# Kernel optimization log

Measured on AMD Instinct MI355X. Metric: run time of the kernel, lower is better.

The kernel has to match this reference:

```python
import jax, jax.numpy as jnp
import numpy as np

N_NODES = 100000
N_EDGES = 1600000
D_FEAT = 128
ALPHA = 0.1
K_STEPS = 10


def setup_inputs() -> dict:
    key = jax.random.key(0)
    k1, k2, k3 = jax.random.split(key, 3)
    x = jax.random.normal(k1, (N_NODES, D_FEAT), dtype=jnp.float32)
    edge_index = jax.random.randint(k2, (2, N_EDGES), 0, N_NODES, dtype=jnp.int64)
    edge_vals = jax.random.uniform(k3, (N_EDGES,), dtype=jnp.float32)
    return {"x": x, "edge_index": edge_index, "edge_vals": edge_vals}


def _spmm(edge_index, edge_vals, h, n_nodes):
    # out[i] = sum_j A[i, j] * h[j]; row = edge_index[0], col = edge_index[1]
    row, col = edge_index[0], edge_index[1]
    msgs = edge_vals[:, None] * h[col]  # [E, d]
    return jax.ops.segment_sum(msgs, row, num_segments=n_nodes)


def reference(x, edge_index, edge_vals):
    # APPNP propagation: h <- (1 - alpha) * A @ h + alpha * x, K steps.
    # dropout=0.0 -> dropout is the identity (as in the torch module default).
    def body(_, h):
        return (1.0 - ALPHA) * _spmm(edge_index, edge_vals, h, N_NODES) + ALPHA * x

    return jax.lax.fori_loop(0, K_STEPS, body, x)
```

## Files before the change

### kernel.cpp

```cpp
#include <hip/hip_runtime.h>


#define N_NODES 100000
#define N_EDGES 1600000
#define D_FEAT  128
#define ALPHA   0.1f
#define K_STEPS 10
#define MAXDEG  64

#define SCAN_ELEMS 512
#define SCAN_NBLK  ((N_NODES + SCAN_ELEMS - 1) / SCAN_ELEMS)

static __device__ __forceinline__ float bf2f(unsigned u16) {
    return __uint_as_float(u16 << 16);
}
static __device__ __forceinline__ unsigned f2bf(float f) {
    unsigned u = __float_as_uint(f);
    return (u + 0x7fffu + ((u >> 16) & 1u)) >> 16;
}


__global__ __launch_bounds__(256) void scatter_padded(const int* __restrict__ rows,
                                                      const int* __restrict__ cols,
                                                      const float* __restrict__ w,
                                                      int* __restrict__ cnt,
                                                      int2* __restrict__ csrp) {
    int e = blockIdx.x * 256 + threadIdx.x;
    if (e < N_EDGES) {
        int r = rows[e];
        int pos = atomicAdd(&cnt[r], 1);
        if (pos < MAXDEG) {
            int2 cw;
            cw.x = cols[e];
            cw.y = __float_as_int((1.0f - ALPHA) * w[e]);
            csrp[((size_t)r << 6) + pos] = cw;
        }
    }
}


__global__ __launch_bounds__(256) void hist_kernel(const int* __restrict__ rows,
                                                   int* __restrict__ deg) {
    int e = blockIdx.x * 256 + threadIdx.x;
    if (e < N_EDGES) atomicAdd(&deg[rows[e]], 1);
}

__global__ __launch_bounds__(256) void scan_partial(const int* __restrict__ deg,
                                                    int* __restrict__ partial) {
    __shared__ int s[256];
    int b = blockIdx.x, t = threadIdx.x;
    int i0 = b * SCAN_ELEMS + t * 2;
    int v0 = (i0 < N_NODES) ? deg[i0] : 0;
    int v1 = (i0 + 1 < N_NODES) ? deg[i0 + 1] : 0;
    s[t] = v0 + v1;
    __syncthreads();
    for (int off = 128; off > 0; off >>= 1) {
        if (t < off) s[t] += s[t + off];
        __syncthreads();
    }
    if (t == 0) partial[b] = s[0];
}

__global__ __launch_bounds__(256) void scan_top(int* __restrict__ partial) {
    __shared__ int s[256];
    int t = threadIdx.x;
    s[t] = (t < SCAN_NBLK) ? partial[t] : 0;
    __syncthreads();
    for (int off = 1; off < 256; off <<= 1) {
        int v = (t >= off) ? s[t - off] : 0;
        __syncthreads();
        s[t] += v;
        __syncthreads();
    }
    if (t < SCAN_NBLK) partial[t] = (t == 0) ? 0 : s[t - 1];
}

__global__ __launch_bounds__(256) void scan_final(int* __restrict__ deg_cursor,
                                                  const int* __restrict__ partial,
                                                  int* __restrict__ row_ptr) {
    __shared__ int s[256];
    int b = blockIdx.x, t = threadIdx.x;
    int i0 = b * SCAN_ELEMS + t * 2;
    int v0 = (i0 < N_NODES) ? deg_cursor[i0] : 0;
    int v1 = (i0 + 1 < N_NODES) ? deg_cursor[i0 + 1] : 0;
    int pair = v0 + v1;
    s[t] = pair;
    __syncthreads();
    for (int off = 1; off < 256; off <<= 1) {
        int v = (t >= off) ? s[t - off] : 0;
        __syncthreads();
        s[t] += v;
        __syncthreads();
    }
    int ex = partial[b] + s[t] - pair;
    if (i0 < N_NODES)     { row_ptr[i0] = ex;          deg_cursor[i0] = ex; }
    if (i0 + 1 < N_NODES) { row_ptr[i0 + 1] = ex + v0; deg_cursor[i0 + 1] = ex + v0; }
    if (b == 0 && t == 0) row_ptr[N_NODES] = N_EDGES;
}

__global__ __launch_bounds__(256) void scatter_kernel(const int* __restrict__ rows,
                                                      const int* __restrict__ cols,
                                                      const float* __restrict__ w,
                                                      int* __restrict__ cursor,
                                                      int2* __restrict__ csr) {
    int e = blockIdx.x * 256 + threadIdx.x;
    if (e < N_EDGES) {
        int pos = atomicAdd(&cursor[rows[e]], 1);
        int2 cw;
        cw.x = cols[e];
        cw.y = __float_as_int((1.0f - ALPHA) * w[e]);
        csr[pos] = cw;
    }
}

__global__ __launch_bounds__(256) void x_to_bf16(const float2* __restrict__ x2,
                                                 unsigned* __restrict__ xb, int n) {
    int i = blockIdx.x * 256 + threadIdx.x;
    if (i < n) {
        float2 v = x2[i];
        xb[i] = f2bf(v.x) | (f2bf(v.y) << 16);
    }
}


template <bool SRC_BF, bool DST_BF, bool X_BF, bool PAD>
__global__ __launch_bounds__(256) void row_spmm_t(const int* __restrict__ rp,
                                                  const int2* __restrict__ csr,
                                                  const void* __restrict__ xsrc,
                                                  const void* __restrict__ src,
                                                  void* __restrict__ dst) {
    int row = (blockIdx.x * 256 + threadIdx.x) >> 6;
    int lane = threadIdx.x & 63;
    if (row >= N_NODES) return;
    int beg, end;
    if (PAD) {
        int cn = rp[row];
        cn = (cn < MAXDEG) ? cn : MAXDEG;
        beg = row << 6;
        end = beg + cn;
    } else {
        beg = rp[row];
        end = rp[row + 1];
    }

    float xtx, xty;
    if (X_BF) {
        unsigned u = ((const unsigned*)xsrc)[(size_t)row * 64 + lane];
        xtx = ALPHA * bf2f(u & 0xffffu);
        xty = ALPHA * bf2f(u >> 16);
    } else {
        float2 xv = ((const float2*)xsrc)[(size_t)row * 64 + lane];
        xtx = ALPHA * xv.x;
        xty = ALPHA * xv.y;
    }

    const float2*   sf = (const float2*)src;
    const unsigned* sb = (const unsigned*)src;

    float ax[4] = {0.f, 0.f, 0.f, 0.f};
    float ay[4] = {0.f, 0.f, 0.f, 0.f};

    auto gather = [&](int col) -> float2 {
        if (SRC_BF) {
            unsigned u = sb[(size_t)col * 64 + lane];
            float2 v;
            v.x = bf2f(u & 0xffffu);
            v.y = bf2f(u >> 16);
            return v;
        } else {
            return sf[(size_t)col * 64 + lane];
        }
    };

    int j = beg;
    while (j + 16 <= end) {
        int2 cw[16];
        #pragma unroll
        for (int u = 0; u < 16; ++u) cw[u] = csr[j + u];
        float2 v[16];
        #pragma unroll
        for (int u = 0; u < 16; ++u) v[u] = gather(cw[u].x);
        #pragma unroll
        for (int u = 0; u < 16; ++u) {
            float wv = __int_as_float(cw[u].y);
            ax[u & 3] += wv * v[u].x;
            ay[u & 3] += wv * v[u].y;
        }
        j += 16;
    }
    while (j + 8 <= end) {
        int2 cw[8];
        #pragma unroll
        for (int u = 0; u < 8; ++u) cw[u] = csr[j + u];
        float2 v[8];
        #pragma unroll
        for (int u = 0; u < 8; ++u) v[u] = gather(cw[u].x);
        #pragma unroll
        for (int u = 0; u < 8; ++u) {
            float wv = __int_as_float(cw[u].y);
            ax[u & 3] += wv * v[u].x;
            ay[u & 3] += wv * v[u].y;
        }
        j += 8;
    }
    while (j + 4 <= end) {
        int2 cw[4];
        #pragma unroll
        for (int u = 0; u < 4; ++u) cw[u] = csr[j + u];
        float2 v[4];
        #pragma unroll
        for (int u = 0; u < 4; ++u) v[u] = gather(cw[u].x);
        #pragma unroll
        for (int u = 0; u < 4; ++u) {
            float wv = __int_as_float(cw[u].y);
            ax[u] += wv * v[u].x;
            ay[u] += wv * v[u].y;
        }
        j += 4;
    }
    for (; j < end; ++j) {
        int2 cw = csr[j];
        float2 v = gather(cw.x);
        float wv = __int_as_float(cw.y);
        ax[0] += wv * v.x;
        ay[0] += wv * v.y;
    }

    float ox = xtx + (ax[0] + ax[1]) + (ax[2] + ax[3]);
    float oy = xty + (ay[0] + ay[1]) + (ay[2] + ay[3]);

    if (DST_BF) {
        ((unsigned*)dst)[(size_t)row * 64 + lane] = f2bf(ox) | (f2bf(oy) << 16);
    } else {
        float2 o; o.x = ox; o.y = oy;
        ((float2*)dst)[(size_t)row * 64 + lane] = o;
    }
}


__global__ __launch_bounds__(256) void init_step(const float4* __restrict__ x,
                                                 float4* __restrict__ dst, int n4) {
    int i = blockIdx.x * 256 + threadIdx.x;
    if (i < n4) {
        float4 v = x[i];
        dst[i] = make_float4(ALPHA * v.x, ALPHA * v.y, ALPHA * v.z, ALPHA * v.w);
    }
}

__global__ __launch_bounds__(256) void edge_scatter(const int* __restrict__ rows,
                                                    const int* __restrict__ cols,
                                                    const float* __restrict__ w,
                                                    const float* __restrict__ h,
                                                    float* __restrict__ dst) {
    unsigned t = blockIdx.x * 256u + threadIdx.x;
    unsigned e = t >> 5;
    unsigned l = t & 31u;
    if (e >= N_EDGES) return;
    int r = rows[e];
    int c = cols[e];
    float we = (1.0f - ALPHA) * w[e];
    const float4* hc = (const float4*)(h + (size_t)c * D_FEAT);
    float4 v = hc[l];
    float* dr = dst + (size_t)r * D_FEAT + (size_t)l * 4;
    unsafeAtomicAdd(dr + 0, we * v.x);
    unsafeAtomicAdd(dr + 1, we * v.y);
    unsafeAtomicAdd(dr + 2, we * v.z);
    unsafeAtomicAdd(dr + 3, we * v.w);
}

extern "C" void kernel_launch(void* const* d_in, const int* in_sizes, int n_in,
                              void* d_out, int out_size, void* d_ws, size_t ws_size,
                              hipStream_t stream) {
    const float* x  = (const float*)d_in[0];
    const int*   ei = (const int*)d_in[1];
    const float* ev = (const float*)d_in[2];
    const int* rows = ei;
    const int* cols = ei + N_EDGES;
    float* out = (float*)d_out;

    auto align16 = [](size_t o) { return (o + 15) & ~(size_t)15; };

    size_t p_off = 0;
    size_t p_ha   = p_off; p_off = align16(p_off + (size_t)N_NODES * D_FEAT * 2);
    size_t p_hb   = p_off; p_off = align16(p_off + (size_t)N_NODES * D_FEAT * 2);
    size_t p_cnt  = p_off; p_off = align16(p_off + (size_t)N_NODES * 4);
    size_t p_csr  = p_off; p_off = align16(p_off + (size_t)N_NODES * MAXDEG * 8);
    size_t p_xb   = p_off; p_off = align16(p_off + (size_t)N_NODES * D_FEAT * 2);
    size_t need_pad = p_off;

    size_t c_off = 0;
    size_t c_ha      = c_off; c_off = align16(c_off + (size_t)N_NODES * D_FEAT * 2);
    size_t c_hb      = c_off; c_off = align16(c_off + (size_t)N_NODES * D_FEAT * 2);
    size_t c_rowptr  = c_off; c_off = align16(c_off + (size_t)(N_NODES + 1) * 4);
    size_t c_cursor  = c_off; c_off = align16(c_off + (size_t)N_NODES * 4);
    size_t c_partial = c_off; c_off = align16(c_off + (size_t)SCAN_NBLK * 4);
    size_t c_csr     = c_off; c_off = align16(c_off + (size_t)N_EDGES * 8);
    size_t need_base = c_off;
    size_t c_xb      = c_off; c_off = align16(c_off + (size_t)N_NODES * D_FEAT * 2);
    size_t need_xb   = c_off;

    const int row_blocks = (N_NODES * 64 + 255) / 256;
    const float2* x2 = (const float2*)x;

    if (ws_size >= need_pad) {
        char* ws = (char*)d_ws;
        void*     h_a  = (void*)(ws + p_ha);
        void*     h_b  = (void*)(ws + p_hb);
        int*      cnt  = (int*)(ws + p_cnt);
        int2*     csrp = (int2*)(ws + p_csr);
        unsigned* xb   = (unsigned*)(ws + p_xb);

        hipMemsetAsync(cnt, 0, (size_t)N_NODES * 4, stream);
        const int edge_blocks_1t = (N_EDGES + 255) / 256;
        scatter_padded<<<edge_blocks_1t, 256, 0, stream>>>(rows, cols, ev, cnt, csrp);

        const int nxb = N_NODES * D_FEAT / 2;
        x_to_bf16<<<(nxb + 255) / 256, 256, 0, stream>>>(x2, xb, nxb);

        row_spmm_t<true, true, true, true><<<row_blocks, 256, 0, stream>>>(
            cnt, csrp, (const void*)xb, (const void*)xb, h_a);
        for (int k = 1; k <= 8; ++k) {
            const void* src = (k & 1) ? h_a : h_b;
            void* dst = (k & 1) ? h_b : h_a;
            row_spmm_t<true, true, true, true><<<row_blocks, 256, 0, stream>>>(
                cnt, csrp, (const void*)xb, src, dst);
        }
        row_spmm_t<true, false, false, true><<<row_blocks, 256, 0, stream>>>(
            cnt, csrp, (const void*)x2, (const void*)h_a, (void*)out);
    } else if (ws_size >= need_base) {
        char* ws = (char*)d_ws;
        void*  h_a     = (void*)(ws + c_ha);
        void*  h_b     = (void*)(ws + c_hb);
        int*   row_ptr = (int*)(ws + c_rowptr);
        int*   cursor  = (int*)(ws + c_cursor);
        int*   partial = (int*)(ws + c_partial);
        int2*  csr     = (int2*)(ws + c_csr);
        unsigned* xb   = (unsigned*)(ws + c_xb);
        const bool has_xb = (ws_size >= need_xb);
        const int edge_blocks_1t = (N_EDGES + 255) / 256;

        hipMemsetAsync(cursor, 0, (size_t)N_NODES * 4, stream);
        hist_kernel<<<edge_blocks_1t, 256, 0, stream>>>(rows, cursor);
        scan_partial<<<SCAN_NBLK, 256, 0, stream>>>(cursor, partial);
        scan_top<<<1, 256, 0, stream>>>(partial);
        scan_final<<<SCAN_NBLK, 256, 0, stream>>>(cursor, partial, row_ptr);
        scatter_kernel<<<edge_blocks_1t, 256, 0, stream>>>(rows, cols, ev, cursor, csr);

        if (has_xb) {
            const int nxb = N_NODES * D_FEAT / 2;
            x_to_bf16<<<(nxb + 255) / 256, 256, 0, stream>>>(x2, xb, nxb);
            row_spmm_t<true, true, true, false><<<row_blocks, 256, 0, stream>>>(
                row_ptr, csr, (const void*)xb, (const void*)xb, h_a);
            for (int k = 1; k <= 8; ++k) {
                const void* src = (k & 1) ? h_a : h_b;
                void* dst = (k & 1) ? h_b : h_a;
                row_spmm_t<true, true, true, false><<<row_blocks, 256, 0, stream>>>(
                    row_ptr, csr, (const void*)xb, src, dst);
            }
            row_spmm_t<true, false, false, false><<<row_blocks, 256, 0, stream>>>(
                row_ptr, csr, (const void*)x2, (const void*)h_a, (void*)out);
        } else {
            row_spmm_t<false, true, false, false><<<row_blocks, 256, 0, stream>>>(
                row_ptr, csr, (const void*)x2, (const void*)x, h_a);
            for (int k = 1; k <= 8; ++k) {
                const void* src = (k & 1) ? h_a : h_b;
                void* dst = (k & 1) ? h_b : h_a;
                row_spmm_t<true, true, false, false><<<row_blocks, 256, 0, stream>>>(
                    row_ptr, csr, (const void*)x2, src, dst);
            }
            row_spmm_t<true, false, false, false><<<row_blocks, 256, 0, stream>>>(
                row_ptr, csr, (const void*)x2, (const void*)h_a, (void*)out);
        }
    } else {
        float* wsf = (float*)d_ws;
        const int n4 = N_NODES * D_FEAT / 4;
        const int init_blocks = (n4 + 255) / 256;
        const int edge_blocks = (N_EDGES * 32 + 255) / 256;
        for (int k = 0; k < K_STEPS; ++k) {
            const float* src = (k == 0) ? x : ((k & 1) ? wsf : out);
            float* dst = (k & 1) ? out : wsf;
            init_step<<<init_blocks, 256, 0, stream>>>((const float4*)x, (float4*)dst, n4);
            edge_scatter<<<edge_blocks, 256, 0, stream>>>(rows, cols, ev, src, dst);
        }
    }
}
```

Measured before the change: 864.6 us.

## Build padded CSR via two-pass shared-memory bucket sort instead of global atomics

Replaces the per-edge global atomicAdd scatter into the padded CSR with two passes. The first groups edges into 512-row buckets using shared-memory histograms and one global atomic per bucket per block. The second has each block place a bucket's edges into rows using shared-memory counters. The goal is to cut contention on global atomics and improve write locality when building the CSR. In exchange it adds an extra round trip through a staging buffer that aliases the h_b and xb workspace, and runs the second pass with only 64 blocks.

```diff
diff --git a/kernel.cpp b/kernel.cpp
--- a/kernel.cpp
+++ b/kernel.cpp
@@ -8,6 +8,10 @@
 #define K_STEPS 10
 #define MAXDEG  64
 
+#define NBUCK 196
+#define BCAP  16000
+#define EPB_A 2048
+
 #define SCAN_ELEMS 512
 #define SCAN_NBLK  ((N_NODES + SCAN_ELEMS - 1) / SCAN_ELEMS)
 
@@ -20,21 +24,79 @@
 }
 
 
-__global__ __launch_bounds__(256) void scatter_padded(const int* __restrict__ rows,
+__global__ __launch_bounds__(256) void bucket_scatter(const int* __restrict__ rows,
                                                       const int* __restrict__ cols,
                                                       const float* __restrict__ w,
-                                                      int* __restrict__ cnt,
-                                                      int2* __restrict__ csrp) {
-    int e = blockIdx.x * 256 + threadIdx.x;
-    if (e < N_EDGES) {
-        int r = rows[e];
-        int pos = atomicAdd(&cnt[r], 1);
-        if (pos < MAXDEG) {
-            int2 cw;
-            cw.x = cols[e];
-            cw.y = __float_as_int((1.0f - ALPHA) * w[e]);
-            csrp[((size_t)r << 6) + pos] = cw;
-        }
+                                                      int* __restrict__ gcount,
+                                                      int4* __restrict__ gbuf) {
+    __shared__ int h_cnt[NBUCK];
+    __shared__ int h_base[NBUCK];
+    __shared__ int h_cur[NBUCK];
+    const int tid = threadIdx.x;
+    for (int i = tid; i < NBUCK; i += 256) { h_cnt[i] = 0; h_cur[i] = 0; }
+    __syncthreads();
+
+    const int base_e = blockIdx.x * EPB_A + tid;
+    int er[8]; int ec[8]; float ew[8];
+    #pragma unroll
+    for (int k = 0; k < 8; ++k) {
+        int e = base_e + k * 256;
+        bool v = (e < N_EDGES);
+        er[k] = v ? rows[e] : -1;
+        ec[k] = v ? cols[e] : 0;
+        ew[k] = v ? w[e] : 0.f;
+        if (v) atomicAdd(&h_cnt[er[k] >> 9], 1);
+    }
+    __syncthreads();
+    for (int i = tid; i < NBUCK; i += 256) {
+        h_base[i] = (h_cnt[i] > 0) ? atomicAdd(&gcount[i], h_cnt[i]) : 0;
+    }
+    __syncthreads();
+    #pragma unroll
+    for (int k = 0; k < 8; ++k) {
+        if (er[k] >= 0) {
+            int b = er[k] >> 9;
+            int p = h_base[b] + atomicAdd(&h_cur[b], 1);
+            if (p < BCAP) {
+                int4 ent;
+                ent.x = er[k];
+                ent.y = ec[k];
+                ent.z = __float_as_int((1.0f - ALPHA) * ew[k]);
+                ent.w = 0;
+                gbuf[(size_t)b * BCAP + p] = ent;
+            }
+        }
+    }
+}
+
+__global__ __launch_bounds__(256) void bucket_to_csr(const int* __restrict__ gcount,
+                                                     const int4* __restrict__ gbuf,
+                                                     int* __restrict__ cnt,
+                                                     int2* __restrict__ csrp) {
+    __shared__ int rcur[512];
+    const int tid = threadIdx.x;
+    for (int b = blockIdx.x; b < NBUCK; b += gridDim.x) {
+        for (int i = tid; i < 512; i += 256) rcur[i] = 0;
+        __syncthreads();
+        int n = gcount[b];
+        if (n > BCAP) n = BCAP;
+        for (int i = tid; i < n; i += 256) {
+            int4 e = gbuf[(size_t)b * BCAP + i];
+            int p = atomicAdd(&rcur[e.x & 511], 1);
+            if (p < MAXDEG) {
+                int2 cw;
+                cw.x = e.y;
+                cw.y = e.z;
+                csrp[((size_t)e.x << 6) + p] = cw;
+            }
+        }
+        __syncthreads();
+        int rowbase = b << 9;
+        for (int i = tid; i < 512; i += 256) {
+            int row = rowbase + i;
+            if (row < N_NODES) cnt[row] = rcur[i];
+        }
+        __syncthreads();
     }
 }
 
@@ -282,11 +344,13 @@
 
     size_t p_off = 0;
     size_t p_ha   = p_off; p_off = align16(p_off + (size_t)N_NODES * D_FEAT * 2);
+    size_t p_cnt  = p_off; p_off = align16(p_off + (size_t)N_NODES * 4 + NBUCK * 4);
+    size_t p_csr  = p_off; p_off = align16(p_off + (size_t)N_NODES * MAXDEG * 8);
     size_t p_hb   = p_off; p_off = align16(p_off + (size_t)N_NODES * D_FEAT * 2);
-    size_t p_cnt  = p_off; p_off = align16(p_off + (size_t)N_NODES * 4);
-    size_t p_csr  = p_off; p_off = align16(p_off + (size_t)N_NODES * MAXDEG * 8);
     size_t p_xb   = p_off; p_off = align16(p_off + (size_t)N_NODES * D_FEAT * 2);
     size_t need_pad = p_off;
+    static_assert((size_t)NBUCK * BCAP * 16 <= 2 * (size_t)N_NODES * D_FEAT * 2,
+                  "gbuf must fit in hb+xb");
 
     size_t c_off = 0;
     size_t c_ha      = c_off; c_off = align16(c_off + (size_t)N_NODES * D_FEAT * 2);
@@ -304,15 +368,18 @@
 
     if (ws_size >= need_pad) {
         char* ws = (char*)d_ws;
-        void*     h_a  = (void*)(ws + p_ha);
-        void*     h_b  = (void*)(ws + p_hb);
-        int*      cnt  = (int*)(ws + p_cnt);
-        int2*     csrp = (int2*)(ws + p_csr);
-        unsigned* xb   = (unsigned*)(ws + p_xb);
-
-        hipMemsetAsync(cnt, 0, (size_t)N_NODES * 4, stream);
-        const int edge_blocks_1t = (N_EDGES + 255) / 256;
-        scatter_padded<<<edge_blocks_1t, 256, 0, stream>>>(rows, cols, ev, cnt, csrp);
+        void*     h_a    = (void*)(ws + p_ha);
+        int*      cnt    = (int*)(ws + p_cnt);
+        int*      gcount = cnt + N_NODES;
+        int2*     csrp   = (int2*)(ws + p_csr);
+        void*     h_b    = (void*)(ws + p_hb);
+        unsigned* xb     = (unsigned*)(ws + p_xb);
+        int4*     gbuf   = (int4*)(ws + p_hb);
+
+        hipMemsetAsync(cnt, 0, (size_t)N_NODES * 4 + NBUCK * 4, stream);
+        const int blocks_a = (N_EDGES + EPB_A - 1) / EPB_A;
+        bucket_scatter<<<blocks_a, 256, 0, stream>>>(rows, cols, ev, gcount, gbuf);
+        bucket_to_csr<<<64, 256, 0, stream>>>(gcount, gbuf, cnt, csrp);
 
         const int nxb = N_NODES * D_FEAT / 2;
         x_to_bf16<<<(nxb + 255) / 256, 256, 0, stream>>>(x2, xb, nxb);
```

Result: slower. 940.5 us (+8.8%).
